# Kernel tuning notes

Measured on AMD Instinct MI355X. Metric: run time of the kernel, lower is better.

## Reference

```python
import jax, jax.numpy as jnp
import numpy as np

NH, HD = 4, 16          # num_heads, head_dim (proj_dim = 64)
SCALE = HD ** -0.5
EPS = 1e-5
G = 16                  # GroupNorm groups = min(16, channels)


def _conv1x1(W, b, x):
    # 1x1 conv == channel-mixing matmul: W (out,in), x (B,in,H,W)
    return jnp.einsum('pc,bchw->bphw', W, x) + b[None, :, None, None]


def _attend(Wq, bq, Wk, bk, Wv, bv, Wo, bo, query, context):
    B, C, H, Wd = query.shape
    N = H * Wd
    q = _conv1x1(Wq, bq, query).astype(jnp.float32).reshape(B, NH, HD, N)
    k = _conv1x1(Wk, bk, context).astype(jnp.float32).reshape(B, NH, HD, N)
    v = _conv1x1(Wv, bv, context).astype(jnp.float32).reshape(B, NH, HD, N)
    attn = jax.nn.softmax(jnp.einsum('bhdn,bhdm->bhnm', q, k) * SCALE, axis=-1)
    out = jnp.einsum('bhdm,bhnm->bhdn', v, attn).reshape(B, NH * HD, H, Wd)
    return _conv1x1(Wo, bo, out)


def _gn(x, gamma, beta):
    B, C, H, W = x.shape
    xr = x.reshape(B, G, C // G, H, W)
    m = xr.mean(axis=(2, 3, 4), keepdims=True)
    v = xr.var(axis=(2, 3, 4), keepdims=True)
    xn = ((xr - m) * jax.lax.rsqrt(v + EPS)).reshape(B, C, H, W)
    return xn * gamma[None, :, None, None] + beta[None, :, None, None]


def setup_inputs() -> dict:
    key = jax.random.key(0)
    C, P, Bn, H, W = 256, 64, 2, 64, 64
    ks = iter(jax.random.split(key, 64))
    d = {}
    for m in ['a', 'b', 'c']:
        d[f'feat_{m}'] = jax.random.normal(next(ks), (Bn, C, H, W), jnp.float32)
    for m in ['a', 'b', 'c']:
        d[f'Wq_{m}'] = 0.02 * jax.random.normal(next(ks), (P, C), jnp.float32)
        d[f'bq_{m}'] = jnp.zeros((P,), jnp.float32)
        d[f'Wk_{m}'] = 0.02 * jax.random.normal(next(ks), (P, 2 * C), jnp.float32)
        d[f'bk_{m}'] = jnp.zeros((P,), jnp.float32)
        d[f'Wv_{m}'] = 0.02 * jax.random.normal(next(ks), (P, 2 * C), jnp.float32)
        d[f'bv_{m}'] = jnp.zeros((P,), jnp.float32)
        d[f'Wo_{m}'] = 0.02 * jax.random.normal(next(ks), (C, P), jnp.float32)
        d[f'bo_{m}'] = jnp.zeros((C,), jnp.float32)
        d[f'g_{m}'] = jnp.ones((C,), jnp.float32)
        d[f'be_{m}'] = jnp.zeros((C,), jnp.float32)
    return d


def reference(feat_a, feat_b, feat_c,
              Wq_a, bq_a, Wk_a, bk_a, Wv_a, bv_a, Wo_a, bo_a, g_a, be_a,
              Wq_b, bq_b, Wk_b, bk_b, Wv_b, bv_b, Wo_b, bo_b, g_b, be_b,
              Wq_c, bq_c, Wk_c, bk_c, Wv_c, bv_c, Wo_c, bo_c, g_c, be_c):
    bc = jnp.concatenate([feat_b, feat_c], axis=1)
    a_out = _gn(feat_a + _attend(Wq_a, bq_a, Wk_a, bk_a, Wv_a, bv_a, Wo_a, bo_a, feat_a, bc), g_a, be_a)
    ac = jnp.concatenate([feat_a, feat_c], axis=1)
    b_out = _gn(feat_b + _attend(Wq_b, bq_b, Wk_b, bk_b, Wv_b, bv_b, Wo_b, bo_b, feat_b, ac), g_b, be_b)
    ab = jnp.concatenate([feat_a, feat_b], axis=1)
    c_out = _gn(feat_c + _attend(Wq_c, bq_c, Wk_c, bk_c, Wv_c, bv_c, Wo_c, bo_c, feat_c, ab), g_c, be_c)
    return (a_out, b_out, c_out)
```

## Files before the change

### kernel.cpp

```cpp
#include <hip/hip_runtime.h>

#define B_ 2
#define C_ 256
#define P_ 64
#define N_ 4096
#define EPS_ 1e-5f
#define QSCALE1024_ 369.32993046757467f

typedef _Float16 half4 __attribute__((ext_vector_type(4)));
typedef _Float16 half8 __attribute__((ext_vector_type(8)));
typedef float f32x4 __attribute__((ext_vector_type(4)));
typedef float f32x16 __attribute__((ext_vector_type(16)));
typedef unsigned int uint4v __attribute__((ext_vector_type(4)));

static __device__ __forceinline__ unsigned int pkexp2(float t0, float t1) {
  unsigned int pk, tmp;
  asm("v_cvt_u32_f32 %0, %2\n\t"
      "v_cvt_u32_f32 %1, %3\n\t"
      "v_cvt_pk_u16_u32 %0, %0, %1"
      : "=&v"(pk), "=&v"(tmp)
      : "v"(t0), "v"(t1));
  return pk;
}

struct TP {
  const float* feat[3];
  const float* Wq[3]; const float* bq[3];
  const float* Wk[3]; const float* bk[3];
  const float* Wv[3]; const float* bv[3];
  const float* Wo[3]; const float* bo[3];
  const float* gm[3]; const float* bt[3];
  _Float16* q16;
  _Float16* k16;
  _Float16* v16;
  _Float16* ao0;
  _Float16* ao1;
  float* L;
  float* stats;
  float* out;
  int ctx0[3]; int ctx1[3];
};

#define PST_ 264
#define VTS_ 88

__global__ __launch_bounds__(256) void proj_fused_kernel(TP P) {
  __shared__ _Float16 bs[64 * PST_];
  const int m = blockIdx.z, b = blockIdx.y;
  const int tid = threadIdx.x;
  const int w = tid >> 6, g = (tid >> 4) & 3, t = tid & 15;
  const bool is_q = blockIdx.x >= 64;
  const int n0 = (is_q ? blockIdx.x - 64 : (int)blockIdx.x) * 64;
  const int sn = tid & 63, scb = (tid >> 6) * 16;

  if (is_q) {
    const float* __restrict__ in = P.feat[m] + (size_t)b * C_ * N_ + n0 + sn;
#pragma unroll
    for (int cc = 0; cc < 4; ++cc) {
      const int c0 = cc * 64 + scb;
      float f[16];
#pragma unroll
      for (int i = 0; i < 16; ++i) f[i] = in[(size_t)(c0 + i) * N_];
      half8 h0, h1;
#pragma unroll
      for (int j = 0; j < 8; ++j) { h0[j] = (_Float16)f[j]; h1[j] = (_Float16)f[8 + j]; }
      *(half8*)(bs + sn * PST_ + c0) = h0;
      *(half8*)(bs + sn * PST_ + c0 + 8) = h1;
    }
    __syncthreads();
    f32x4 a[4] = {{0.f,0.f,0.f,0.f},{0.f,0.f,0.f,0.f},{0.f,0.f,0.f,0.f},{0.f,0.f,0.f,0.f}};
    const float* __restrict__ Wq = P.Wq[m] + (w * 16 + t) * 256;
#pragma unroll
    for (int ks = 0; ks < 8; ++ks) {
      const float4 wa = *(const float4*)(Wq + ks * 32 + g * 8);
      const float4 wb = *(const float4*)(Wq + ks * 32 + g * 8 + 4);
      half8 af;
      af[0] = (_Float16)wa.x; af[1] = (_Float16)wa.y;
      af[2] = (_Float16)wa.z; af[3] = (_Float16)wa.w;
      af[4] = (_Float16)wb.x; af[5] = (_Float16)wb.y;
      af[6] = (_Float16)wb.z; af[7] = (_Float16)wb.w;
#pragma unroll
      for (int i = 0; i < 4; ++i) {
        const half8 bf = *(const half8*)(bs + (i * 16 + t) * PST_ + ks * 32 + g * 8);
        a[i] = __builtin_amdgcn_mfma_f32_16x16x32_f16(af, bf, a[i], 0, 0, 0);
      }
    }
    float bq[4];
#pragma unroll
    for (int r = 0; r < 4; ++r) bq[r] = P.bq[m][w * 16 + g * 4 + r];
    _Float16* qo = P.q16 + ((size_t)(m * 2 + b) * N_) * 64 + w * 16 + g * 4;
#pragma unroll
    for (int i = 0; i < 4; ++i) {
      half4 hq;
#pragma unroll
      for (int r = 0; r < 4; ++r) hq[r] = (_Float16)((a[i][r] + bq[r]) * QSCALE1024_);
      *(half4*)(qo + (size_t)(n0 + i * 16 + t) * 64) = hq;
    }
  } else {
    f32x4 ka[4] = {{0.f,0.f,0.f,0.f},{0.f,0.f,0.f,0.f},{0.f,0.f,0.f,0.f},{0.f,0.f,0.f,0.f}};
    f32x4 va[4] = {{0.f,0.f,0.f,0.f},{0.f,0.f,0.f,0.f},{0.f,0.f,0.f,0.f},{0.f,0.f,0.f,0.f}};
    const int srcs[2] = {P.ctx0[m], P.ctx1[m]};
    for (int src = 0; src < 2; ++src) {
      const float* __restrict__ in =
          P.feat[srcs[src]] + (size_t)b * C_ * N_ + n0 + sn;
      if (src) __syncthreads();
#pragma unroll
      for (int cc = 0; cc < 4; ++cc) {
        const int c0 = cc * 64 + scb;
        float f[16];
#pragma unroll
        for (int i = 0; i < 16; ++i) f[i] = in[(size_t)(c0 + i) * N_];
        half8 h0, h1;
#pragma unroll
        for (int j = 0; j < 8; ++j) { h0[j] = (_Float16)f[j]; h1[j] = (_Float16)f[8 + j]; }
        *(half8*)(bs + sn * PST_ + c0) = h0;
        *(half8*)(bs + sn * PST_ + c0 + 8) = h1;
      }
      __syncthreads();
      const float* __restrict__ Wk = P.Wk[m] + (w * 16 + t) * 512 + src * 256;
      const float* __restrict__ Wv = P.Wv[m] + (w * 16 + t) * 512 + src * 256;
#pragma unroll
      for (int ks = 0; ks < 8; ++ks) {
        const float4 k0 = *(const float4*)(Wk + ks * 32 + g * 8);
        const float4 k1 = *(const float4*)(Wk + ks * 32 + g * 8 + 4);
        const float4 v0 = *(const float4*)(Wv + ks * 32 + g * 8);
        const float4 v1 = *(const float4*)(Wv + ks * 32 + g * 8 + 4);
        half8 ak, av;
        ak[0] = (_Float16)k0.x; ak[1] = (_Float16)k0.y;
        ak[2] = (_Float16)k0.z; ak[3] = (_Float16)k0.w;
        ak[4] = (_Float16)k1.x; ak[5] = (_Float16)k1.y;
        ak[6] = (_Float16)k1.z; ak[7] = (_Float16)k1.w;
        av[0] = (_Float16)v0.x; av[1] = (_Float16)v0.y;
        av[2] = (_Float16)v0.z; av[3] = (_Float16)v0.w;
        av[4] = (_Float16)v1.x; av[5] = (_Float16)v1.y;
        av[6] = (_Float16)v1.z; av[7] = (_Float16)v1.w;
#pragma unroll
        for (int i = 0; i < 4; ++i) {
          const half8 bf = *(const half8*)(bs + (i * 16 + t) * PST_ + ks * 32 + g * 8);
          ka[i] = __builtin_amdgcn_mfma_f32_16x16x32_f16(ak, bf, ka[i], 0, 0, 0);
          va[i] = __builtin_amdgcn_mfma_f32_16x16x32_f16(av, bf, va[i], 0, 0, 0);
        }
      }
    }
    float bk[4], bv[4];
#pragma unroll
    for (int r = 0; r < 4; ++r) {
      bk[r] = P.bk[m][w * 16 + g * 4 + r];
      bv[r] = P.bv[m][w * 16 + g * 4 + r];
    }
    _Float16* ko = P.k16 + ((size_t)(m * 8 + b * 4 + w) * N_) * 16 + g * 4;
#pragma unroll
    for (int i = 0; i < 4; ++i) {
      half4 hk;
#pragma unroll
      for (int r = 0; r < 4; ++r) hk[r] = (_Float16)(ka[i][r] + bk[r]);
      *(half4*)(ko + (size_t)(n0 + i * 16 + t) * 16) = hk;
    }
    __syncthreads();
#pragma unroll
    for (int i = 0; i < 4; ++i)
#pragma unroll
      for (int r = 0; r < 4; ++r)
        bs[(w * 16 + g * 4 + r) * VTS_ + i * 16 + t] = (_Float16)(va[i][r] + bv[r]);
    __syncthreads();
#pragma unroll
    for (int pass = 0; pass < 2; ++pass) {
      const int row = pass * 32 + (tid >> 3);
      const int hh = row >> 4, dd = row & 15, nb = (tid & 7) * 8;
      const half8 hv = *(const half8*)(bs + row * VTS_ + nb);
      *(half8*)(P.v16 + ((size_t)(m * 8 + b * 4 + hh) * 16 + dd) * N_ + n0 + nb) = hv;
    }
  }
}

#define KST_ 24
#define VST_ 264

__global__ __launch_bounds__(512) void attn_kernel(TP P) {
  const int m = blockIdx.z, bh = blockIdx.y;
  const int tid = threadIdx.x;
  if (m == 0 && bh == 0 && blockIdx.x == 0 && tid < 192) P.stats[tid] = 0.f;
  const int kvh = blockIdx.x & 1, qb = blockIdx.x >> 1;
  const int kvbase = kvh * 2048;
  const int w = tid >> 6;
  const int lane = tid & 63;
  const int n = lane & 31;
  const int hh = lane >> 5;
  const int b = bh >> 2, h = bh & 3;
  const _Float16* __restrict__ kh = P.k16 + ((size_t)(m * 8 + bh) * N_) * 16;
  const _Float16* __restrict__ vh = P.v16 + ((size_t)(m * 8 + bh) * 16) * N_;
  const int q0 = qb * 256 + w * 32;
  const half8 qf = *(const half8*)(P.q16 +
      ((size_t)(m * 2 + b) * N_ + q0 + n) * 64 + h * 16 + hh * 8);

  __shared__ _Float16 ks[256 * KST_];
  __shared__ _Float16 vs[32 * VST_];

  if (tid < 32) {
    half8 o8;
#pragma unroll
    for (int j = 0; j < 8; ++j) o8[j] = (_Float16)1.0f;
    *(half8*)(vs + 16 * VST_ + tid * 8) = o8;
  }

  const int kr = tid >> 1, kc8 = tid & 1;
  const int vr = tid >> 5, vc = tid & 31;
  const _Float16* kgp = kh + (size_t)(kvbase + kr) * 16 + kc8 * 8;
  const _Float16* vgp = vh + (size_t)vr * N_ + kvbase + vc * 8;
  _Float16* ksp = ks + kr * KST_ + kc8 * 8;
  _Float16* vsp = vs + vr * VST_ + vc * 8;

  half8 kpre = *(const half8*)kgp;
  half8 vpre = *(const half8*)vgp;

  f32x16 Z, Oe, Oo;
#pragma unroll
  for (int r = 0; r < 16; ++r) { Z[r] = 15360.5f; Oe[r] = 0.f; Oo[r] = 0.f; }

  for (int c0 = 0; c0 < 2048; c0 += 256) {
    *(half8*)ksp = kpre;
    *(half8*)vsp = vpre;
    __syncthreads();
    const int nxt = (c0 + 256 < 2048) ? c0 + 256 : 0;
    kpre = *(const half8*)(kgp + (size_t)nxt * 16);
    vpre = *(const half8*)(vgp + nxt);
#pragma unroll
    for (int sub = 0; sub < 8; ++sub) {
      const half8 kf = *(const half8*)(ks + (sub * 32 + n) * KST_ + hh * 8);
      const f32x16 s = __builtin_amdgcn_mfma_f32_32x32x16_f16(kf, qf, Z, 0, 0, 0);
      unsigned int p0 = pkexp2(s[0], s[1]);
      unsigned int p1 = pkexp2(s[2], s[3]);
      unsigned int p2 = pkexp2(s[4], s[5]);
      unsigned int p3 = pkexp2(s[6], s[7]);
      unsigned int p4 = pkexp2(s[8], s[9]);
      unsigned int p5 = pkexp2(s[10], s[11]);
      unsigned int p6 = pkexp2(s[12], s[13]);
      unsigned int p7 = pkexp2(s[14], s[15]);
      asm("v_permlane32_swap_b32 %0, %1" : "+v"(p2), "+v"(p0));
      asm("v_permlane32_swap_b32 %0, %1" : "+v"(p3), "+v"(p1));
      asm("v_permlane32_swap_b32 %0, %1" : "+v"(p6), "+v"(p4));
      asm("v_permlane32_swap_b32 %0, %1" : "+v"(p7), "+v"(p5));
      const uint4v ua = {p0, p1, p2, p3};
      const uint4v ub = {p4, p5, p6, p7};
      const half8 ve = *(const half8*)(vs + n * VST_ + sub * 32 + hh * 8);
      const half8 vo = *(const half8*)(vs + n * VST_ + sub * 32 + 16 + hh * 8);
      Oe = __builtin_amdgcn_mfma_f32_32x32x16_f16(
          __builtin_bit_cast(half8, ua), ve, Oe, 0, 0, 0);
      Oo = __builtin_amdgcn_mfma_f32_32x32x16_f16(
          __builtin_bit_cast(half8, ub), vo, Oo, 0, 0, 0);
    }
    __syncthreads();
  }

  if (n < 16) {
    _Float16* aop = (kvh ? P.ao1 : P.ao0) +
                    ((size_t)(m * 2 + b) * N_ + q0) * 64 + h * 16 + n;
#pragma unroll
    for (int r = 0; r < 16; ++r) {
      const int qrow = (r & 3) + 8 * (r >> 2) + 4 * hh;
      aop[(size_t)qrow * 64] = (_Float16)(Oe[r] + Oo[r]);
    }
  } else if (n == 16) {
    float* Lp = P.L + ((size_t)(kvh * 3 + m) * 8 + bh) * N_ + q0;
#pragma unroll
    for (int r = 0; r < 16; ++r) {
      const int qrow = (r & 3) + 8 * (r >> 2) + 4 * hh;
      Lp[qrow] = Oe[r] + Oo[r];
    }
  }
}

#define BS_ 72

__global__ __launch_bounds__(256) void wo_resid_kernel(TP P) {
  __shared__ _Float16 as[64 * BS_];
  const int m = blockIdx.z;
  const int b = blockIdx.y >> 2, cblk = blockIdx.y & 3;
  const int n0 = blockIdx.x * 64;
  const int tid = threadIdx.x;
  const int w = tid >> 6, g = (tid >> 4) & 3, t = tid & 15;
  const int c0 = cblk * 64 + w * 16;
  const size_t aob = ((size_t)(m * 2 + b) * N_) * 64;
  const _Float16* __restrict__ a0p = P.ao0 + aob;
  const _Float16* __restrict__ a1p = P.ao1 + aob;
  const int ar = tid >> 2, ac = (tid & 3) * 16;
  {
    const size_t off = (size_t)(n0 + ar) * 64 + ac;
    half8 s0 = *(const half8*)(a0p + off);
    half8 s1 = *(const half8*)(a0p + off + 8);
    const half8 u0 = *(const half8*)(a1p + off);
    const half8 u1 = *(const half8*)(a1p + off + 8);
#pragma unroll
    for (int r = 0; r < 8; ++r) { s0[r] += u0[r]; s1[r] += u1[r]; }
    *(half8*)(as + ar * BS_ + ac) = s0;
    *(half8*)(as + ar * BS_ + ac + 8) = s1;
  }
  __syncthreads();
  const float* __restrict__ L0 = P.L + ((size_t)m * 8 + b * 4) * N_;
  const float* __restrict__ L1 = P.L + ((size_t)(3 + m) * 8 + b * 4) * N_;
  f32x4 acc[4] = {{0.f,0.f,0.f,0.f},{0.f,0.f,0.f,0.f},{0.f,0.f,0.f,0.f},{0.f,0.f,0.f,0.f}};
  const float* __restrict__ Wo = P.Wo[m] + (c0 + t) * 64;
#pragma unroll
  for (int kst = 0; kst < 2; ++kst) {
    const float4 w0 = *(const float4*)(Wo + kst * 32 + g * 8);
    const float4 w1 = *(const float4*)(Wo + kst * 32 + g * 8 + 4);
    half8 a;
    a[0] = (_Float16)w0.x; a[1] = (_Float16)w0.y;
    a[2] = (_Float16)w0.z; a[3] = (_Float16)w0.w;
    a[4] = (_Float16)w1.x; a[5] = (_Float16)w1.y;
    a[6] = (_Float16)w1.z; a[7] = (_Float16)w1.w;
    const int head = kst * 2 + (g >> 1);
#pragma unroll
    for (int i = 0; i < 4; ++i) {
      const int nn = n0 + i * 16 + t;
      half8 bf = *(const half8*)(as + (i * 16 + t) * BS_ + kst * 32 + g * 8);
      const float ls = L0[(size_t)head * N_ + nn] + L1[(size_t)head * N_ + nn];
      const _Float16 hs = (_Float16)(1.0f / ls);
#pragma unroll
      for (int r = 0; r < 8; ++r) bf[r] *= hs;
      acc[i] = __builtin_amdgcn_mfma_f32_16x16x32_f16(a, bf, acc[i], 0, 0, 0);
    }
  }
  const float* __restrict__ X = P.feat[m] + (size_t)b * C_ * N_;
  float* outb = P.out + (size_t)m * B_ * C_ * N_ + (size_t)b * C_ * N_;
  float s = 0.f, s2 = 0.f;
#pragma unroll
  for (int i = 0; i < 4; ++i) {
    const int nn = n0 + i * 16 + t;
#pragma unroll
    for (int r = 0; r < 4; ++r) {
      const int c = c0 + g * 4 + r;
      const float val = acc[i][r] + X[(size_t)c * N_ + nn] + P.bo[m][c];
      outb[(size_t)c * N_ + nn] = val;
      s += val;
      s2 += val * val;
    }
  }
#pragma unroll
  for (int off = 1; off < 64; off <<= 1) {
    s += __shfl_xor(s, off);
    s2 += __shfl_xor(s2, off);
  }
  if ((tid & 63) == 0) {
    const int group = cblk * 4 + w;
    float* st = P.stats + ((size_t)(m * 2 + b) * 16 + group) * 2;
    atomicAdd(st, s);
    atomicAdd(st + 1, s2);
  }
}

__global__ __launch_bounds__(256) void gn_final_kernel(TP P) {
  const size_t base = ((size_t)blockIdx.x * 256 + threadIdx.x) * 4;
#pragma unroll
  for (int it = 0; it < 4; ++it) {
    const size_t idx = base + (size_t)it * 1572864;
    const int m = (int)(idx >> 21);
    const int rem = (int)(idx & ((1u << 21) - 1));
    const int b = rem >> 20;
    const int c = (rem >> 12) & 255;
    const float* st = P.stats + ((size_t)(m * 2 + b) * 16 + (c >> 4)) * 2;
    const float mean = st[0] * (1.f / 65536.f);
    const float var = st[1] * (1.f / 65536.f) - mean * mean;
    const float rstd = rsqrtf(var + EPS_);
    const float ga = P.gm[m][c] * rstd, be = P.bt[m][c];
    float4 x = *(float4*)(P.out + idx);
    x.x = (x.x - mean) * ga + be;
    x.y = (x.y - mean) * ga + be;
    x.z = (x.z - mean) * ga + be;
    x.w = (x.w - mean) * ga + be;
    *(float4*)(P.out + idx) = x;
  }
}

extern "C" void kernel_launch(void* const* d_in, const int* in_sizes, int n_in,
                              void* d_out, int out_size, void* d_ws, size_t ws_size,
                              hipStream_t stream) {
  TP P;
  for (int m = 0; m < 3; ++m) {
    P.feat[m] = (const float*)d_in[m];
    const int base = 3 + m * 10;
    P.Wq[m] = (const float*)d_in[base + 0];
    P.bq[m] = (const float*)d_in[base + 1];
    P.Wk[m] = (const float*)d_in[base + 2];
    P.bk[m] = (const float*)d_in[base + 3];
    P.Wv[m] = (const float*)d_in[base + 4];
    P.bv[m] = (const float*)d_in[base + 5];
    P.Wo[m] = (const float*)d_in[base + 6];
    P.bo[m] = (const float*)d_in[base + 7];
    P.gm[m] = (const float*)d_in[base + 8];
    P.bt[m] = (const float*)d_in[base + 9];
  }
  _Float16* ws = (_Float16*)d_ws;
  P.q16 = ws;
  P.k16 = ws + 1572864;
  P.v16 = ws + 3145728;
  P.ao0 = ws + 4718592;
  P.ao1 = ws + 6291456;
  P.L = (float*)(ws + 7864320);
  P.stats = (float*)(ws + 7864320) + 196608;
  P.out = (float*)d_out;
  P.ctx0[0] = 1; P.ctx1[0] = 2;
  P.ctx0[1] = 0; P.ctx1[1] = 2;
  P.ctx0[2] = 0; P.ctx1[2] = 1;

  proj_fused_kernel<<<dim3(128, 2, 3), dim3(256), 0, stream>>>(P);
  attn_kernel<<<dim3(32, 8, 3), dim3(512), 0, stream>>>(P);
  wo_resid_kernel<<<dim3(64, 8, 3), dim3(256), 0, stream>>>(P);
  gn_final_kernel<<<dim3(1536), dim3(256), 0, stream>>>(P);
}
```

Measured before the change: 252.4 us.

## Process two query tiles per attention wave and hoist loads in epilogue kernels

The attention kernel moves from 512 threads with one 32-query tile per wave to 256 threads with two 32-query tiles per wave. Each K fragment and V fragment read from shared memory now feeds two sets of MFMAs, which halves LDS traffic per unit of work and gives more independent MFMA/exp work to interleave, at the cost of more accumulator registers. The Wo/residual kernel issues its global loads (L, Wo, bias, residual X) early so they overlap the LDS staging and barrier. The GroupNorm finalize kernel now uses one float4 per thread across a 4x larger grid.

```diff
diff --git a/kernel.cpp b/kernel.cpp
--- a/kernel.cpp
+++ b/kernel.cpp
@@ -176,7 +176,7 @@
 #define KST_ 24
 #define VST_ 264
 
-__global__ __launch_bounds__(512) void attn_kernel(TP P) {
+__global__ __launch_bounds__(256) void attn_kernel(TP P) {
   const int m = blockIdx.z, bh = blockIdx.y;
   const int tid = threadIdx.x;
   if (m == 0 && bh == 0 && blockIdx.x == 0 && tid < 192) P.stats[tid] = 0.f;
@@ -189,9 +189,10 @@
   const int b = bh >> 2, h = bh & 3;
   const _Float16* __restrict__ kh = P.k16 + ((size_t)(m * 8 + bh) * N_) * 16;
   const _Float16* __restrict__ vh = P.v16 + ((size_t)(m * 8 + bh) * 16) * N_;
-  const int q0 = qb * 256 + w * 32;
-  const half8 qf = *(const half8*)(P.q16 +
-      ((size_t)(m * 2 + b) * N_ + q0 + n) * 64 + h * 16 + hh * 8);
+  const int q0b = qb * 256 + w * 64;
+  const _Float16* qbase = P.q16 + ((size_t)(m * 2 + b) * N_ + q0b + n) * 64 + h * 16 + hh * 8;
+  const half8 qf0 = *(const half8*)qbase;
+  const half8 qf1 = *(const half8*)(qbase + 32 * 64);
 
   __shared__ _Float16 ks[256 * KST_];
   __shared__ _Float16 vs[32 * VST_];
@@ -203,69 +204,105 @@
     *(half8*)(vs + 16 * VST_ + tid * 8) = o8;
   }
 
-  const int kr = tid >> 1, kc8 = tid & 1;
-  const int vr = tid >> 5, vc = tid & 31;
-  const _Float16* kgp = kh + (size_t)(kvbase + kr) * 16 + kc8 * 8;
-  const _Float16* vgp = vh + (size_t)vr * N_ + kvbase + vc * 8;
-  _Float16* ksp = ks + kr * KST_ + kc8 * 8;
-  _Float16* vsp = vs + vr * VST_ + vc * 8;
-
-  half8 kpre = *(const half8*)kgp;
-  half8 vpre = *(const half8*)vgp;
-
-  f32x16 Z, Oe, Oo;
-#pragma unroll
-  for (int r = 0; r < 16; ++r) { Z[r] = 15360.5f; Oe[r] = 0.f; Oo[r] = 0.f; }
+  const int vr = tid >> 4, vcc = tid & 15;
+  const _Float16* kgp = kh + (size_t)(kvbase + tid) * 16;
+  const _Float16* vgp = vh + (size_t)vr * N_ + kvbase + vcc * 16;
+  _Float16* ksp = ks + tid * KST_;
+  _Float16* vsp = vs + vr * VST_ + vcc * 16;
+
+  half8 kpre0 = *(const half8*)kgp;
+  half8 kpre1 = *(const half8*)(kgp + 8);
+  half8 vpre0 = *(const half8*)vgp;
+  half8 vpre1 = *(const half8*)(vgp + 8);
+
+  f32x16 Z, Oe0, Oo0, Oe1, Oo1;
+#pragma unroll
+  for (int r = 0; r < 16; ++r) {
+    Z[r] = 15360.5f; Oe0[r] = 0.f; Oo0[r] = 0.f; Oe1[r] = 0.f; Oo1[r] = 0.f;
+  }
 
   for (int c0 = 0; c0 < 2048; c0 += 256) {
-    *(half8*)ksp = kpre;
-    *(half8*)vsp = vpre;
+    *(half8*)ksp = kpre0;
+    *(half8*)(ksp + 8) = kpre1;
+    *(half8*)vsp = vpre0;
+    *(half8*)(vsp + 8) = vpre1;
     __syncthreads();
     const int nxt = (c0 + 256 < 2048) ? c0 + 256 : 0;
-    kpre = *(const half8*)(kgp + (size_t)nxt * 16);
-    vpre = *(const half8*)(vgp + nxt);
+    kpre0 = *(const half8*)(kgp + (size_t)nxt * 16);
+    kpre1 = *(const half8*)(kgp + (size_t)nxt * 16 + 8);
+    vpre0 = *(const half8*)(vgp + nxt);
+    vpre1 = *(const half8*)(vgp + nxt + 8);
 #pragma unroll
     for (int sub = 0; sub < 8; ++sub) {
       const half8 kf = *(const half8*)(ks + (sub * 32 + n) * KST_ + hh * 8);
-      const f32x16 s = __builtin_amdgcn_mfma_f32_32x32x16_f16(kf, qf, Z, 0, 0, 0);
-      unsigned int p0 = pkexp2(s[0], s[1]);
-      unsigned int p1 = pkexp2(s[2], s[3]);
-      unsigned int p2 = pkexp2(s[4], s[5]);
-      unsigned int p3 = pkexp2(s[6], s[7]);
-      unsigned int p4 = pkexp2(s[8], s[9]);
-      unsigned int p5 = pkexp2(s[10], s[11]);
-      unsigned int p6 = pkexp2(s[12], s[13]);
-      unsigned int p7 = pkexp2(s[14], s[15]);
-      asm("v_permlane32_swap_b32 %0, %1" : "+v"(p2), "+v"(p0));
-      asm("v_permlane32_swap_b32 %0, %1" : "+v"(p3), "+v"(p1));
-      asm("v_permlane32_swap_b32 %0, %1" : "+v"(p6), "+v"(p4));
-      asm("v_permlane32_swap_b32 %0, %1" : "+v"(p7), "+v"(p5));
-      const uint4v ua = {p0, p1, p2, p3};
-      const uint4v ub = {p4, p5, p6, p7};
+      const f32x16 s0 = __builtin_amdgcn_mfma_f32_32x32x16_f16(kf, qf0, Z, 0, 0, 0);
+      const f32x16 s1 = __builtin_amdgcn_mfma_f32_32x32x16_f16(kf, qf1, Z, 0, 0, 0);
       const half8 ve = *(const half8*)(vs + n * VST_ + sub * 32 + hh * 8);
       const half8 vo = *(const half8*)(vs + n * VST_ + sub * 32 + 16 + hh * 8);
-      Oe = __builtin_amdgcn_mfma_f32_32x32x16_f16(
-          __builtin_bit_cast(half8, ua), ve, Oe, 0, 0, 0);
-      Oo = __builtin_amdgcn_mfma_f32_32x32x16_f16(
-          __builtin_bit_cast(half8, ub), vo, Oo, 0, 0, 0);
+      {
+        unsigned int p0 = pkexp2(s0[0], s0[1]);
+        unsigned int p1 = pkexp2(s0[2], s0[3]);
+        unsigned int p2 = pkexp2(s0[4], s0[5]);
+        unsigned int p3 = pkexp2(s0[6], s0[7]);
+        unsigned int p4 = pkexp2(s0[8], s0[9]);
+        unsigned int p5 = pkexp2(s0[10], s0[11]);
+        unsigned int p6 = pkexp2(s0[12], s0[13]);
+        unsigned int p7 = pkexp2(s0[14], s0[15]);
+        asm("v_permlane32_swap_b32 %0, %1" : "+v"(p2), "+v"(p0));
+        asm("v_permlane32_swap_b32 %0, %1" : "+v"(p3), "+v"(p1));
+        asm("v_permlane32_swap_b32 %0, %1" : "+v"(p6), "+v"(p4));
+        asm("v_permlane32_swap_b32 %0, %1" : "+v"(p7), "+v"(p5));
+        const uint4v ua = {p0, p1, p2, p3};
+        const uint4v ub = {p4, p5, p6, p7};
+        Oe0 = __builtin_amdgcn_mfma_f32_32x32x16_f16(
+            __builtin_bit_cast(half8, ua), ve, Oe0, 0, 0, 0);
+        Oo0 = __builtin_amdgcn_mfma_f32_32x32x16_f16(
+            __builtin_bit_cast(half8, ub), vo, Oo0, 0, 0, 0);
+      }
+      {
+        unsigned int p0 = pkexp2(s1[0], s1[1]);
+        unsigned int p1 = pkexp2(s1[2], s1[3]);
+        unsigned int p2 = pkexp2(s1[4], s1[5]);
+        unsigned int p3 = pkexp2(s1[6], s1[7]);
+        unsigned int p4 = pkexp2(s1[8], s1[9]);
+        unsigned int p5 = pkexp2(s1[10], s1[11]);
+        unsigned int p6 = pkexp2(s1[12], s1[13]);
+        unsigned int p7 = pkexp2(s1[14], s1[15]);
+        asm("v_permlane32_swap_b32 %0, %1" : "+v"(p2), "+v"(p0));
+        asm("v_permlane32_swap_b32 %0, %1" : "+v"(p3), "+v"(p1));
+        asm("v_permlane32_swap_b32 %0, %1" : "+v"(p6), "+v"(p4));
+        asm("v_permlane32_swap_b32 %0, %1" : "+v"(p7), "+v"(p5));
+        const uint4v ua = {p0, p1, p2, p3};
+        const uint4v ub = {p4, p5, p6, p7};
+        Oe1 = __builtin_amdgcn_mfma_f32_32x32x16_f16(
+            __builtin_bit_cast(half8, ua), ve, Oe1, 0, 0, 0);
+        Oo1 = __builtin_amdgcn_mfma_f32_32x32x16_f16(
+            __builtin_bit_cast(half8, ub), vo, Oo1, 0, 0, 0);
+      }
     }
     __syncthreads();
   }
 
-  if (n < 16) {
-    _Float16* aop = (kvh ? P.ao1 : P.ao0) +
-                    ((size_t)(m * 2 + b) * N_ + q0) * 64 + h * 16 + n;
-#pragma unroll
-    for (int r = 0; r < 16; ++r) {
-      const int qrow = (r & 3) + 8 * (r >> 2) + 4 * hh;
-      aop[(size_t)qrow * 64] = (_Float16)(Oe[r] + Oo[r]);
-    }
-  } else if (n == 16) {
-    float* Lp = P.L + ((size_t)(kvh * 3 + m) * 8 + bh) * N_ + q0;
-#pragma unroll
-    for (int r = 0; r < 16; ++r) {
-      const int qrow = (r & 3) + 8 * (r >> 2) + 4 * hh;
-      Lp[qrow] = Oe[r] + Oo[r];
+#pragma unroll
+  for (int qg = 0; qg < 2; ++qg) {
+    const int q0 = q0b + qg * 32;
+    const f32x16& Oe = qg ? Oe1 : Oe0;
+    const f32x16& Oo = qg ? Oo1 : Oo0;
+    if (n < 16) {
+      _Float16* aop = (kvh ? P.ao1 : P.ao0) +
+                      ((size_t)(m * 2 + b) * N_ + q0) * 64 + h * 16 + n;
+#pragma unroll
+      for (int r = 0; r < 16; ++r) {
+        const int qrow = (r & 3) + 8 * (r >> 2) + 4 * hh;
+        aop[(size_t)qrow * 64] = (_Float16)(Oe[r] + Oo[r]);
+      }
+    } else if (n == 16) {
+      float* Lp = P.L + ((size_t)(kvh * 3 + m) * 8 + bh) * N_ + q0;
+#pragma unroll
+      for (int r = 0; r < 16; ++r) {
+        const int qrow = (r & 3) + 8 * (r >> 2) + 4 * hh;
+        Lp[qrow] = Oe[r] + Oo[r];
+      }
     }
   }
 }
@@ -283,45 +320,77 @@
   const size_t aob = ((size_t)(m * 2 + b) * N_) * 64;
   const _Float16* __restrict__ a0p = P.ao0 + aob;
   const _Float16* __restrict__ a1p = P.ao1 + aob;
+
   const int ar = tid >> 2, ac = (tid & 3) * 16;
-  {
-    const size_t off = (size_t)(n0 + ar) * 64 + ac;
-    half8 s0 = *(const half8*)(a0p + off);
-    half8 s1 = *(const half8*)(a0p + off + 8);
-    const half8 u0 = *(const half8*)(a1p + off);
-    const half8 u1 = *(const half8*)(a1p + off + 8);
-#pragma unroll
-    for (int r = 0; r < 8; ++r) { s0[r] += u0[r]; s1[r] += u1[r]; }
-    *(half8*)(as + ar * BS_ + ac) = s0;
-    *(half8*)(as + ar * BS_ + ac + 8) = s1;
-  }
-  __syncthreads();
+  const size_t off = (size_t)(n0 + ar) * 64 + ac;
+  half8 s0 = *(const half8*)(a0p + off);
+  half8 s1 = *(const half8*)(a0p + off + 8);
+  const half8 u0 = *(const half8*)(a1p + off);
+  const half8 u1 = *(const half8*)(a1p + off + 8);
+
   const float* __restrict__ L0 = P.L + ((size_t)m * 8 + b * 4) * N_;
   const float* __restrict__ L1 = P.L + ((size_t)(3 + m) * 8 + b * 4) * N_;
-  f32x4 acc[4] = {{0.f,0.f,0.f,0.f},{0.f,0.f,0.f,0.f},{0.f,0.f,0.f,0.f},{0.f,0.f,0.f,0.f}};
-  const float* __restrict__ Wo = P.Wo[m] + (c0 + t) * 64;
+  float l0v[2][4], l1v[2][4];
 #pragma unroll
   for (int kst = 0; kst < 2; ++kst) {
-    const float4 w0 = *(const float4*)(Wo + kst * 32 + g * 8);
-    const float4 w1 = *(const float4*)(Wo + kst * 32 + g * 8 + 4);
-    half8 a;
-    a[0] = (_Float16)w0.x; a[1] = (_Float16)w0.y;
-    a[2] = (_Float16)w0.z; a[3] = (_Float16)w0.w;
-    a[4] = (_Float16)w1.x; a[5] = (_Float16)w1.y;
-    a[6] = (_Float16)w1.z; a[7] = (_Float16)w1.w;
     const int head = kst * 2 + (g >> 1);
 #pragma unroll
     for (int i = 0; i < 4; ++i) {
       const int nn = n0 + i * 16 + t;
+      l0v[kst][i] = L0[(size_t)head * N_ + nn];
+      l1v[kst][i] = L1[(size_t)head * N_ + nn];
+    }
+  }
+  const float* __restrict__ Wo = P.Wo[m] + (c0 + t) * 64;
+  float4 wv0[2], wv1[2];
+#pragma unroll
+  for (int kst = 0; kst < 2; ++kst) {
+    wv0[kst] = *(const float4*)(Wo + kst * 32 + g * 8);
+    wv1[kst] = *(const float4*)(Wo + kst * 32 + g * 8 + 4);
+  }
+  float bov[4];
+#pragma unroll
+  for (int r = 0; r < 4; ++r) bov[r] = P.bo[m][c0 + g * 4 + r];
+
+#pragma unroll
+  for (int r = 0; r < 8; ++r) { s0[r] += u0[r]; s1[r] += u1[r]; }
+  *(half8*)(as + ar * BS_ + ac) = s0;
+  *(half8*)(as + ar * BS_ + ac + 8) = s1;
+  __syncthreads();
+
+  _Float16 hsv[2][4];
+#pragma unroll
+  for (int kst = 0; kst < 2; ++kst)
+#pragma unroll
+    for (int i = 0; i < 4; ++i)
+      hsv[kst][i] = (_Float16)(1.0f / (l0v[kst][i] + l1v[kst][i]));
+
+  f32x4 acc[4] = {{0.f,0.f,0.f,0.f},{0.f,0.f,0.f,0.f},{0.f,0.f,0.f,0.f},{0.f,0.f,0.f,0.f}};
+#pragma unroll
+  for (int kst = 0; kst < 2; ++kst) {
+    half8 a;
+    a[0] = (_Float16)wv0[kst].x; a[1] = (_Float16)wv0[kst].y;
+    a[2] = (_Float16)wv0[kst].z; a[3] = (_Float16)wv0[kst].w;
+    a[4] = (_Float16)wv1[kst].x; a[5] = (_Float16)wv1[kst].y;
+    a[6] = (_Float16)wv1[kst].z; a[7] = (_Float16)wv1[kst].w;
+#pragma unroll
+    for (int i = 0; i < 4; ++i) {
       half8 bf = *(const half8*)(as + (i * 16 + t) * BS_ + kst * 32 + g * 8);
-      const float ls = L0[(size_t)head * N_ + nn] + L1[(size_t)head * N_ + nn];
-      const _Float16 hs = (_Float16)(1.0f / ls);
+      const _Float16 hs = hsv[kst][i];
 #pragma unroll
       for (int r = 0; r < 8; ++r) bf[r] *= hs;
       acc[i] = __builtin_amdgcn_mfma_f32_16x16x32_f16(a, bf, acc[i], 0, 0, 0);
     }
   }
   const float* __restrict__ X = P.feat[m] + (size_t)b * C_ * N_;
+  float xv[4][4];
+#pragma unroll
+  for (int i = 0; i < 4; ++i) {
+    const int nn = n0 + i * 16 + t;
+#pragma unroll
+    for (int r = 0; r < 4; ++r)
+      xv[i][r] = X[(size_t)(c0 + g * 4 + r) * N_ + nn];
+  }
   float* outb = P.out + (size_t)m * B_ * C_ * N_ + (size_t)b * C_ * N_;
   float s = 0.f, s2 = 0.f;
 #pragma unroll
@@ -329,17 +398,16 @@
     const int nn = n0 + i * 16 + t;
 #pragma unroll
     for (int r = 0; r < 4; ++r) {
-      const int c = c0 + g * 4 + r;
-      const float val = acc[i][r] + X[(size_t)c * N_ + nn] + P.bo[m][c];
-      outb[(size_t)c * N_ + nn] = val;
+      const float val = acc[i][r] + xv[i][r] + bov[r];
+      outb[(size_t)(c0 + g * 4 + r) * N_ + nn] = val;
       s += val;
       s2 += val * val;
     }
   }
 #pragma unroll
-  for (int off = 1; off < 64; off <<= 1) {
-    s += __shfl_xor(s, off);
-    s2 += __shfl_xor(s2, off);
+  for (int offd = 1; offd < 64; offd <<= 1) {
+    s += __shfl_xor(s, offd);
+    s2 += __shfl_xor(s2, offd);
   }
   if ((tid & 63) == 0) {
     const int group = cblk * 4 + w;
@@ -350,26 +418,24 @@
 }
 
 __global__ __launch_bounds__(256) void gn_final_kernel(TP P) {
-  const size_t base = ((size_t)blockIdx.x * 256 + threadIdx.x) * 4;
-#pragma unroll
-  for (int it = 0; it < 4; ++it) {
-    const size_t idx = base + (size_t)it * 1572864;
-    const int m = (int)(idx >> 21);
-    const int rem = (int)(idx & ((1u << 21) - 1));
-    const int b = rem >> 20;
-    const int c = (rem >> 12) & 255;
-    const float* st = P.stats + ((size_t)(m * 2 + b) * 16 + (c >> 4)) * 2;
-    const float mean = st[0] * (1.f / 65536.f);
-    const float var = st[1] * (1.f / 65536.f) - mean * mean;
-    const float rstd = rsqrtf(var + EPS_);
-    const float ga = P.gm[m][c] * rstd, be = P.bt[m][c];
-    float4 x = *(float4*)(P.out + idx);
-    x.x = (x.x - mean) * ga + be;
-    x.y = (x.y - mean) * ga + be;
-    x.z = (x.z - mean) * ga + be;
-    x.w = (x.w - mean) * ga + be;
-    *(float4*)(P.out + idx) = x;
-  }
+  const size_t idx = ((size_t)blockIdx.x * 256 + threadIdx.x) * 4;
+  const int m = (int)(idx >> 21);
+  const int rem = (int)(idx & ((1u << 21) - 1));
+  const int b = rem >> 20;
+  const int c = (rem >> 12) & 255;
+  const float* st = P.stats + ((size_t)(m * 2 + b) * 16 + (c >> 4)) * 2;
+  const float s0 = st[0];
+  const float s1 = st[1];
+  float4 x = *(float4*)(P.out + idx);
+  const float mean = s0 * (1.f / 65536.f);
+  const float var = s1 * (1.f / 65536.f) - mean * mean;
+  const float rstd = rsqrtf(var + EPS_);
+  const float ga = P.gm[m][c] * rstd, be = P.bt[m][c];
+  x.x = (x.x - mean) * ga + be;
+  x.y = (x.y - mean) * ga + be;
+  x.z = (x.z - mean) * ga + be;
+  x.w = (x.w - mean) * ga + be;
+  *(float4*)(P.out + idx) = x;
 }
 
 extern "C" void kernel_launch(void* const* d_in, const int* in_sizes, int n_in,
@@ -404,7 +470,7 @@
   P.ctx0[2] = 0; P.ctx1[2] = 1;
 
   proj_fused_kernel<<<dim3(128, 2, 3), dim3(256), 0, stream>>>(P);
-  attn_kernel<<<dim3(32, 8, 3), dim3(512), 0, stream>>>(P);
+  attn_kernel<<<dim3(32, 8, 3), dim3(256), 0, stream>>>(P);
   wo_resid_kernel<<<dim3(64, 8, 3), dim3(256), 0, stream>>>(P);
-  gn_final_kernel<<<dim3(1536), dim3(256), 0, stream>>>(P);
-}
+  gn_final_kernel<<<dim3(6144), dim3(256), 0, stream>>>(P);
+}
```

After: 264.6 us. +4.8%, slower.
